# Optimization experiments

Hardware: AMD Instinct MI355X
Metric: run time of the kernel (lower is better)

Reference implementation:

```python
import jax, jax.numpy as jnp
import numpy as np

IN_FEATURES = 256
OUT_FEATURES = 256
GRID_SIZE = 5
SPLINE_ORDER = 3
GRID_RANGE = (-1.0, 1.0)
LN_EPS = 1e-5


def _make_grid():
    h = (GRID_RANGE[1] - GRID_RANGE[0]) / GRID_SIZE
    n_knots = GRID_SIZE + 2 * SPLINE_ORDER + 1  # 12
    return jnp.linspace(GRID_RANGE[0] - h * SPLINE_ORDER,
                        GRID_RANGE[1] + h * SPLINE_ORDER,
                        n_knots, dtype=jnp.float32)


def setup_inputs() -> dict:
    key = jax.random.key(0)
    k1, k2, k3 = jax.random.split(key, 3)
    N = 65536
    # kaiming_uniform_(nonlinearity='linear'): bound = sqrt(3/fan_in)
    b1 = np.sqrt(3.0 / IN_FEATURES)
    fan_sp = IN_FEATURES * (GRID_SIZE + SPLINE_ORDER)
    b2 = np.sqrt(3.0 / fan_sp)
    return {
        "x": jax.random.normal(k1, (N, IN_FEATURES), dtype=jnp.float32),
        "grid": _make_grid(),
        "base_weight": jax.random.uniform(k2, (OUT_FEATURES, IN_FEATURES), jnp.float32, -b1, b1),
        "spline_weight": jax.random.uniform(k3, (OUT_FEATURES, IN_FEATURES, GRID_SIZE + SPLINE_ORDER), jnp.float32, -b2, b2),
        "ln_gamma": jnp.ones((OUT_FEATURES,), jnp.float32),
        "ln_beta": jnp.zeros((OUT_FEATURES,), jnp.float32),
        "prelu_a": jnp.full((1,), 0.25, jnp.float32),
    }


def reference(x, grid, base_weight, spline_weight, ln_gamma, ln_beta, prelu_a):
    # base branch: exact GELU then linear (matches nn.GELU() + F.linear)
    base_out = jnp.einsum('ni,oi->no', jax.nn.gelu(x, approximate=False), base_weight)

    # Cox-de Boor B-spline basis recursion. grid is identical per feature in
    # the original ([in, 12] expand of a 1D linspace) so we broadcast the 1D grid.
    xu = x[:, :, None]                                   # [N, in, 1]
    bases = ((xu >= grid[:-1]) & (xu < grid[1:])).astype(x.dtype)  # [N, in, 11]
    for k in range(1, SPLINE_ORDER + 1):
        left = grid[:-(k + 1)]
        right = grid[k:-1]
        delta = jnp.where(right == left, jnp.ones_like(right), right - left)
        bases = ((xu - left) / delta * bases[:, :, :-1]
                 + (grid[k + 1:] - xu) / (grid[k + 1:] - grid[1:-k]) * bases[:, :, 1:])
    # bases: [N, in, grid_size + spline_order]

    spline_out = jnp.einsum('nig,oig->no', bases, spline_weight)

    y = base_out + spline_out
    mu = jnp.mean(y, axis=-1, keepdims=True)
    var = jnp.mean(jnp.square(y - mu), axis=-1, keepdims=True)
    y = (y - mu) * jax.lax.rsqrt(var + LN_EPS) * ln_gamma + ln_beta
    # PReLU with a single shared slope (nn.PReLU default)
    return jnp.where(y >= 0, y, prelu_a[0] * y)
```

## Files before the change

### kernel.cpp

```cpp
#include <hip/hip_runtime.h>
#include <hip/hip_bf16.h>
#include <math.h>
#include <stdint.h>

typedef __attribute__((ext_vector_type(8))) short short8;
typedef __attribute__((ext_vector_type(8))) unsigned short u16x8;
typedef __attribute__((ext_vector_type(4))) float f32x4;

#define BM 256
#define BK 64
#define NKT 36
#define A_BYTES (BM * 128)
#define W_BYTES (256 * 128)
#define LDS_TOTAL (2 * A_BYTES + 2 * W_BYTES)

__device__ __forceinline__ unsigned short f2bf(float f) {
    union { float f; unsigned u; } c; c.f = f;
    unsigned u = c.u;
    unsigned r = u + 0x7fffu + ((u >> 16) & 1u);
    return (unsigned short)(r >> 16);
}

__device__ __forceinline__ float gelu_exact(float x) {
    return 0.5f * x * (1.0f + erff(x * 0.7071067811865475f));
}

__device__ __forceinline__ int swz(int row, int u) {
    return row * 128 + ((u ^ (row & 7)) << 4);
}

__global__ void kan_prep_w(const float* __restrict__ bw, const float* __restrict__ sw,
                           unsigned short* __restrict__ Ws) {
    int U = blockIdx.x * 256 + threadIdx.x;
    if (U >= NKT * 2048) return;
    int kt = U >> 11, lu = U & 2047;
    int row = lu >> 3, s = lu & 7;
    int uu = s ^ (row & 7);
    int k = kt * 64 + uu * 8;
    u16x8 pk;
#pragma unroll
    for (int e = 0; e < 8; ++e) {
        int kk = k + e;
        float v = (kk < 256) ? bw[row * 256 + kk] : sw[row * 2048 + (kk - 256)];
        pk[e] = f2bf(v);
    }
    *(u16x8*)(Ws + (size_t)U * 8) = pk;
}

__device__ __forceinline__ void w_issue(int kt, unsigned char* ldsWbuf,
                                        const unsigned short* __restrict__ Wshuf,
                                        int wid, int lane) {
    const unsigned short* wsrc = Wshuf + ((size_t)kt * 2048 + wid * 256 + lane) * 8;
    unsigned char* wdst = ldsWbuf + wid * 4096;
#pragma unroll
    for (int r = 0; r < 4; ++r) {
        __builtin_amdgcn_global_load_lds(
            (const __attribute__((address_space(1))) void*)(wsrc + r * 512),
            (__attribute__((address_space(3))) void*)(wdst + r * 1024),
            16, 0, 0);
    }
}

__device__ __forceinline__ u16x8 spline_row(float xv) {
    float xi = (xv + 2.2f) * 2.5f;
    float fi = floorf(xi);
    float tt = xi - fi;
    float s1 = 1.0f - tt;
    float t2 = tt * tt, t3 = t2 * tt;
    float w0 = s1 * s1 * s1 * (1.0f / 6.0f);
    float w1 = 0.5f * t3 - t2 + (2.0f / 3.0f);
    float w2 = -0.5f * t3 + 0.5f * t2 + 0.5f * tt + (1.0f / 6.0f);
    float w3 = t3 * (1.0f / 6.0f);
    uint64_t Wp = (uint64_t)f2bf(w0) | ((uint64_t)f2bf(w1) << 16)
                | ((uint64_t)f2bf(w2) << 32) | ((uint64_t)f2bf(w3) << 48);
    int b = 16 * ((int)fi - 3);
    uint64_t L = (b >= 0 && b < 64) ? (Wp << b)
               : ((b < 0 && b > -64) ? (Wp >> (-b)) : 0ull);
    uint64_t H = (b >= 64 && b < 128) ? (Wp << (b - 64))
               : ((b > 0 && b < 64) ? (Wp >> (64 - b)) : 0ull);
    union { uint64_t q[2]; u16x8 v; } rr;
    rr.q[0] = L; rr.q[1] = H;
    return rr.v;
}

__global__ __launch_bounds__(512, 2) void kan_fused(
    const float* __restrict__ X, const unsigned short* __restrict__ Wshuf,
    const float* __restrict__ gamma, const float* __restrict__ beta,
    const float* __restrict__ prelu_a, float* __restrict__ OUT)
{
    extern __shared__ __align__(16) unsigned char lds[];

    const int t = threadIdx.x;
    const int row0 = blockIdx.x * BM;
    const int wid = t >> 6, lane = t & 63;
    const int wr = wid >> 2, wc = wid & 3;
    const int lcol = lane & 15, q = lane >> 4;
    const int srow = t >> 3, scol = t & 7;

    f32x4 acc[8][4];
#pragma unroll
    for (int m = 0; m < 8; ++m)
#pragma unroll
        for (int n = 0; n < 4; ++n) acc[m][n] = (f32x4){0.f, 0.f, 0.f, 0.f};

    w_issue(0, lds + 2 * A_BYTES, Wshuf, wid, lane);
    {
        float xg[32];
#pragma unroll
        for (int rep = 0; rep < 4; ++rep) {
            const float* xp = X + (size_t)(row0 + srow + rep * 64) * 256 + scol * 8;
            float4 v0 = *(const float4*)xp;
            float4 v1 = *(const float4*)(xp + 4);
            xg[rep * 8 + 0] = v0.x; xg[rep * 8 + 1] = v0.y; xg[rep * 8 + 2] = v0.z; xg[rep * 8 + 3] = v0.w;
            xg[rep * 8 + 4] = v1.x; xg[rep * 8 + 5] = v1.y; xg[rep * 8 + 6] = v1.z; xg[rep * 8 + 7] = v1.w;
        }
#pragma unroll
        for (int rep = 0; rep < 4; ++rep) {
            u16x8 pk;
#pragma unroll
            for (int j = 0; j < 8; ++j) pk[j] = f2bf(gelu_exact(xg[rep * 8 + j]));
            *(u16x8*)(lds + swz(srow + rep * 64, scol)) = pk;
        }
    }
    __syncthreads();

    for (int kt = 0; kt < NKT; ++kt) {
        const int cur = kt & 1;
        unsigned char* A_cur = lds + cur * A_BYTES;
        unsigned char* W_cur = lds + 2 * A_BYTES + cur * W_BYTES;
        unsigned char* A_nxt = lds + (cur ^ 1) * A_BYTES;
        unsigned char* W_nxt = lds + 2 * A_BYTES + (cur ^ 1) * W_BYTES;
        const bool has_next = (kt + 1 < NKT);
        const bool nxt_gelu = (kt + 1 < 4);

        float xg[32]; float xs[4];
        if (has_next) {
            if (nxt_gelu) {
#pragma unroll
                for (int rep = 0; rep < 4; ++rep) {
                    const float* xp = X + (size_t)(row0 + srow + rep * 64) * 256
                                    + (kt + 1) * 64 + scol * 8;
                    float4 v0 = *(const float4*)xp;
                    float4 v1 = *(const float4*)(xp + 4);
                    xg[rep * 8 + 0] = v0.x; xg[rep * 8 + 1] = v0.y; xg[rep * 8 + 2] = v0.z; xg[rep * 8 + 3] = v0.w;
                    xg[rep * 8 + 4] = v1.x; xg[rep * 8 + 5] = v1.y; xg[rep * 8 + 6] = v1.z; xg[rep * 8 + 7] = v1.w;
                }
            } else {
                const int ibase = (kt + 1 - 4) * 8;
#pragma unroll
                for (int rep = 0; rep < 4; ++rep)
                    xs[rep] = X[(size_t)(row0 + srow + rep * 64) * 256 + ibase + scol];
            }
            w_issue(kt + 1, W_nxt, Wshuf, wid, lane);
        }

        short8 af[8], bfr[4];
#pragma unroll
        for (int m = 0; m < 8; ++m)
            af[m] = *(const short8*)(A_cur + swz(wr * 128 + m * 16 + lcol, q));
#pragma unroll
        for (int n = 0; n < 4; ++n)
            bfr[n] = *(const short8*)(W_cur + swz(wc * 64 + n * 16 + lcol, q));
#pragma unroll
        for (int m = 0; m < 8; ++m)
#pragma unroll
            for (int n = 0; n < 4; ++n)
                acc[m][n] = __builtin_amdgcn_mfma_f32_16x16x32_bf16(
                    af[m], bfr[n], acc[m][n], 0, 0, 0);
#pragma unroll
        for (int m = 0; m < 8; ++m)
            af[m] = *(const short8*)(A_cur + swz(wr * 128 + m * 16 + lcol, 4 + q));
#pragma unroll
        for (int n = 0; n < 4; ++n)
            bfr[n] = *(const short8*)(W_cur + swz(wc * 64 + n * 16 + lcol, 4 + q));
#pragma unroll
        for (int m = 0; m < 8; ++m)
#pragma unroll
            for (int n = 0; n < 4; ++n)
                acc[m][n] = __builtin_amdgcn_mfma_f32_16x16x32_bf16(
                    af[m], bfr[n], acc[m][n], 0, 0, 0);

        if (has_next) {
            if (nxt_gelu) {
#pragma unroll
                for (int rep = 0; rep < 4; ++rep) {
                    u16x8 pk;
#pragma unroll
                    for (int j = 0; j < 8; ++j) pk[j] = f2bf(gelu_exact(xg[rep * 8 + j]));
                    *(u16x8*)(A_nxt + swz(srow + rep * 64, scol)) = pk;
                }
            } else {
#pragma unroll
                for (int rep = 0; rep < 4; ++rep)
                    *(u16x8*)(A_nxt + swz(srow + rep * 64, scol)) = spline_row(xs[rep]);
            }
        }
        __syncthreads();
    }

    float* stats = (float*)lds;
#pragma unroll
    for (int m = 0; m < 8; ++m) {
#pragma unroll
        for (int r = 0; r < 4; ++r) {
            float s = 0.f, s2 = 0.f;
#pragma unroll
            for (int n = 0; n < 4; ++n) { float v = acc[m][n][r]; s += v; s2 += v * v; }
#pragma unroll
            for (int msk = 1; msk < 16; msk <<= 1) {
                s  += __shfl_xor(s,  msk, 64);
                s2 += __shfl_xor(s2, msk, 64);
            }
            if ((lane & 15) == ((m * 4 + r) & 15)) {
                int row = wr * 128 + m * 16 + q * 4 + r;
                stats[row * 8 + wc]     = s;
                stats[row * 8 + 4 + wc] = s2;
            }
        }
    }
    __syncthreads();

    const float apr = prelu_a[0];
    float gv[4], bv[4];
#pragma unroll
    for (int n = 0; n < 4; ++n) {
        int col = wc * 64 + n * 16 + lcol;
        gv[n] = gamma[col]; bv[n] = beta[col];
    }
#pragma unroll
    for (int m = 0; m < 8; ++m) {
#pragma unroll
        for (int r = 0; r < 4; ++r) {
            int row = wr * 128 + m * 16 + q * 4 + r;
            f32x4 sv = *(const f32x4*)(stats + row * 8);
            f32x4 qv = *(const f32x4*)(stats + row * 8 + 4);
            float mu  = (sv[0] + sv[1] + sv[2] + sv[3]) * (1.0f / 256.0f);
            float ex2 = (qv[0] + qv[1] + qv[2] + qv[3]) * (1.0f / 256.0f);
            float rs = rsqrtf(ex2 - mu * mu + 1e-5f);
            float* op = OUT + (size_t)(row0 + row) * 256;
#pragma unroll
            for (int n = 0; n < 4; ++n) {
                int col = wc * 64 + n * 16 + lcol;
                float y = (acc[m][n][r] - mu) * rs * gv[n] + bv[n];
                op[col] = (y >= 0.f) ? y : apr * y;
            }
        }
    }
}

extern "C" void kernel_launch(void* const* d_in, const int* in_sizes, int n_in,
                              void* d_out, int out_size, void* d_ws, size_t ws_size,
                              hipStream_t stream) {
    const float* x  = (const float*)d_in[0];
    const float* bw = (const float*)d_in[2];
    const float* sw = (const float*)d_in[3];
    const float* g  = (const float*)d_in[4];
    const float* be = (const float*)d_in[5];
    const float* pa = (const float*)d_in[6];
    float* out = (float*)d_out;
    unsigned short* Ws = (unsigned short*)d_ws;

    hipFuncSetAttribute((const void*)kan_fused,
                        hipFuncAttributeMaxDynamicSharedMemorySize, LDS_TOTAL);

    const int Nrows = in_sizes[0] / 256;
    kan_prep_w<<<(NKT * 2048 + 255) / 256, 256, 0, stream>>>(bw, sw, Ws);
    kan_fused<<<Nrows / BM, 512, LDS_TOTAL, stream>>>(x, Ws, g, be, pa, out);
}
```

Before: 136.4 us.

## Load weight fragments directly into registers, dropping LDS staging for W

The prep kernel now writes weights in MFMA fragment order, so each wave loads its B operands straight from global memory into registers, double-buffered across k-tiles. The W LDS buffers and the global_load_lds path are removed, which halves LDS use and removes the B-side LDS reads. __syncthreads is replaced by a raw lgkmcnt wait plus s_barrier. The costs are more register pressure (16 short8 buffers on top of 32 accumulators) and a global-load latency sitting inside each iteration. The raw barrier does not wait on vmcnt, so correctness depends on the compiler placing waits before the register-held weights are used.

```diff
diff --git a/kernel.cpp b/kernel.cpp
--- a/kernel.cpp
+++ b/kernel.cpp
@@ -4,15 +4,12 @@
 #include <stdint.h>
 
 typedef __attribute__((ext_vector_type(8))) short short8;
-typedef __attribute__((ext_vector_type(8))) unsigned short u16x8;
 typedef __attribute__((ext_vector_type(4))) float f32x4;
 
 #define BM 256
-#define BK 64
 #define NKT 36
 #define A_BYTES (BM * 128)
-#define W_BYTES (256 * 128)
-#define LDS_TOTAL (2 * A_BYTES + 2 * W_BYTES)
+#define LDS_TOTAL (2 * A_BYTES)
 
 __device__ __forceinline__ unsigned short f2bf(float f) {
     union { float f; unsigned u; } c; c.f = f;
@@ -30,38 +27,26 @@
 }
 
 __global__ void kan_prep_w(const float* __restrict__ bw, const float* __restrict__ sw,
-                           unsigned short* __restrict__ Ws) {
+                           unsigned short* __restrict__ Wf) {
     int U = blockIdx.x * 256 + threadIdx.x;
     if (U >= NKT * 2048) return;
-    int kt = U >> 11, lu = U & 2047;
-    int row = lu >> 3, s = lu & 7;
-    int uu = s ^ (row & 7);
-    int k = kt * 64 + uu * 8;
-    u16x8 pk;
+    int kt = U >> 11, rem = U & 2047;
+    int wcq = rem >> 9, rem2 = rem & 511;
+    int i = rem2 >> 6;
+    int lane = rem2 & 63;
+    int o = wcq * 64 + (i & 3) * 16 + (lane & 15);
+    int k0 = kt * 64 + ((i >> 2) * 4 + (lane >> 4)) * 8;
+    unsigned short pk[8];
 #pragma unroll
     for (int e = 0; e < 8; ++e) {
-        int kk = k + e;
-        float v = (kk < 256) ? bw[row * 256 + kk] : sw[row * 2048 + (kk - 256)];
+        int kk = k0 + e;
+        float v = (kk < 256) ? bw[o * 256 + kk] : sw[o * 2048 + (kk - 256)];
         pk[e] = f2bf(v);
     }
-    *(u16x8*)(Ws + (size_t)U * 8) = pk;
-}
-
-__device__ __forceinline__ void w_issue(int kt, unsigned char* ldsWbuf,
-                                        const unsigned short* __restrict__ Wshuf,
-                                        int wid, int lane) {
-    const unsigned short* wsrc = Wshuf + ((size_t)kt * 2048 + wid * 256 + lane) * 8;
-    unsigned char* wdst = ldsWbuf + wid * 4096;
-#pragma unroll
-    for (int r = 0; r < 4; ++r) {
-        __builtin_amdgcn_global_load_lds(
-            (const __attribute__((address_space(1))) void*)(wsrc + r * 512),
-            (__attribute__((address_space(3))) void*)(wdst + r * 1024),
-            16, 0, 0);
-    }
-}
-
-__device__ __forceinline__ u16x8 spline_row(float xv) {
+    *(short8*)(Wf + (size_t)U * 8) = *(short8*)pk;
+}
+
+__device__ __forceinline__ short8 spline_row(float xv) {
     float xi = (xv + 2.2f) * 2.5f;
     float fi = floorf(xi);
     float tt = xi - fi;
@@ -78,13 +63,13 @@
                : ((b < 0 && b > -64) ? (Wp >> (-b)) : 0ull);
     uint64_t H = (b >= 64 && b < 128) ? (Wp << (b - 64))
                : ((b > 0 && b < 64) ? (Wp >> (64 - b)) : 0ull);
-    union { uint64_t q[2]; u16x8 v; } rr;
+    union { uint64_t q[2]; short8 v; } rr;
     rr.q[0] = L; rr.q[1] = H;
     return rr.v;
 }
 
 __global__ __launch_bounds__(512, 2) void kan_fused(
-    const float* __restrict__ X, const unsigned short* __restrict__ Wshuf,
+    const float* __restrict__ X, const unsigned short* __restrict__ Wf,
     const float* __restrict__ gamma, const float* __restrict__ beta,
     const float* __restrict__ prelu_a, float* __restrict__ OUT)
 {
@@ -103,33 +88,30 @@
 #pragma unroll
         for (int n = 0; n < 4; ++n) acc[m][n] = (f32x4){0.f, 0.f, 0.f, 0.f};
 
-    w_issue(0, lds + 2 * A_BYTES, Wshuf, wid, lane);
+    const unsigned short* wlane = Wf + ((size_t)wc * 512 + lane) * 8;
+
+    short8 wvA[8], wvB[8];
+#pragma unroll
+    for (int i = 0; i < 8; ++i)
+        wvA[i] = *(const short8*)(wlane + i * 512);
     {
-        float xg[32];
 #pragma unroll
         for (int rep = 0; rep < 4; ++rep) {
             const float* xp = X + (size_t)(row0 + srow + rep * 64) * 256 + scol * 8;
             float4 v0 = *(const float4*)xp;
             float4 v1 = *(const float4*)(xp + 4);
-            xg[rep * 8 + 0] = v0.x; xg[rep * 8 + 1] = v0.y; xg[rep * 8 + 2] = v0.z; xg[rep * 8 + 3] = v0.w;
-            xg[rep * 8 + 4] = v1.x; xg[rep * 8 + 5] = v1.y; xg[rep * 8 + 6] = v1.z; xg[rep * 8 + 7] = v1.w;
-        }
-#pragma unroll
-        for (int rep = 0; rep < 4; ++rep) {
-            u16x8 pk;
-#pragma unroll
-            for (int j = 0; j < 8; ++j) pk[j] = f2bf(gelu_exact(xg[rep * 8 + j]));
-            *(u16x8*)(lds + swz(srow + rep * 64, scol)) = pk;
-        }
-    }
-    __syncthreads();
-
-    for (int kt = 0; kt < NKT; ++kt) {
-        const int cur = kt & 1;
-        unsigned char* A_cur = lds + cur * A_BYTES;
-        unsigned char* W_cur = lds + 2 * A_BYTES + cur * W_BYTES;
-        unsigned char* A_nxt = lds + (cur ^ 1) * A_BYTES;
-        unsigned char* W_nxt = lds + 2 * A_BYTES + (cur ^ 1) * W_BYTES;
+            float vv[8] = {v0.x, v0.y, v0.z, v0.w, v1.x, v1.y, v1.z, v1.w};
+            unsigned short pk[8];
+#pragma unroll
+            for (int j = 0; j < 8; ++j) pk[j] = f2bf(gelu_exact(vv[j]));
+            *(short8*)(lds + swz(srow + rep * 64, scol)) = *(short8*)pk;
+        }
+    }
+    asm volatile("s_waitcnt lgkmcnt(0)\n\ts_barrier" ::: "memory");
+
+    auto body = [&](int kt, short8 (&wv)[8], short8 (&wn)[8]) {
+        unsigned char* A_cur = lds + (kt & 1) * A_BYTES;
+        unsigned char* A_nxt = lds + ((kt + 1) & 1) * A_BYTES;
         const bool has_next = (kt + 1 < NKT);
         const bool nxt_gelu = (kt + 1 < 4);
 
@@ -142,8 +124,10 @@
                                     + (kt + 1) * 64 + scol * 8;
                     float4 v0 = *(const float4*)xp;
                     float4 v1 = *(const float4*)(xp + 4);
-                    xg[rep * 8 + 0] = v0.x; xg[rep * 8 + 1] = v0.y; xg[rep * 8 + 2] = v0.z; xg[rep * 8 + 3] = v0.w;
-                    xg[rep * 8 + 4] = v1.x; xg[rep * 8 + 5] = v1.y; xg[rep * 8 + 6] = v1.z; xg[rep * 8 + 7] = v1.w;
+                    xg[rep * 8 + 0] = v0.x; xg[rep * 8 + 1] = v0.y;
+                    xg[rep * 8 + 2] = v0.z; xg[rep * 8 + 3] = v0.w;
+                    xg[rep * 8 + 4] = v1.x; xg[rep * 8 + 5] = v1.y;
+                    xg[rep * 8 + 6] = v1.z; xg[rep * 8 + 7] = v1.w;
                 }
             } else {
                 const int ibase = (kt + 1 - 4) * 8;
@@ -151,51 +135,47 @@
                 for (int rep = 0; rep < 4; ++rep)
                     xs[rep] = X[(size_t)(row0 + srow + rep * 64) * 256 + ibase + scol];
             }
-            w_issue(kt + 1, W_nxt, Wshuf, wid, lane);
-        }
-
-        short8 af[8], bfr[4];
-#pragma unroll
-        for (int m = 0; m < 8; ++m)
-            af[m] = *(const short8*)(A_cur + swz(wr * 128 + m * 16 + lcol, q));
-#pragma unroll
-        for (int n = 0; n < 4; ++n)
-            bfr[n] = *(const short8*)(W_cur + swz(wc * 64 + n * 16 + lcol, q));
-#pragma unroll
-        for (int m = 0; m < 8; ++m)
-#pragma unroll
-            for (int n = 0; n < 4; ++n)
-                acc[m][n] = __builtin_amdgcn_mfma_f32_16x16x32_bf16(
-                    af[m], bfr[n], acc[m][n], 0, 0, 0);
-#pragma unroll
-        for (int m = 0; m < 8; ++m)
-            af[m] = *(const short8*)(A_cur + swz(wr * 128 + m * 16 + lcol, 4 + q));
-#pragma unroll
-        for (int n = 0; n < 4; ++n)
-            bfr[n] = *(const short8*)(W_cur + swz(wc * 64 + n * 16 + lcol, 4 + q));
-#pragma unroll
-        for (int m = 0; m < 8; ++m)
-#pragma unroll
-            for (int n = 0; n < 4; ++n)
-                acc[m][n] = __builtin_amdgcn_mfma_f32_16x16x32_bf16(
-                    af[m], bfr[n], acc[m][n], 0, 0, 0);
+            const unsigned short* wsrc = wlane + (size_t)(kt + 1) * 2048 * 8;
+#pragma unroll
+            for (int i = 0; i < 8; ++i)
+                wn[i] = *(const short8*)(wsrc + i * 512);
+        }
+
+#pragma unroll
+        for (int kh = 0; kh < 2; ++kh) {
+            short8 af[8];
+#pragma unroll
+            for (int m = 0; m < 8; ++m)
+                af[m] = *(const short8*)(A_cur + swz(wr * 128 + m * 16 + lcol, kh * 4 + q));
+#pragma unroll
+            for (int m = 0; m < 8; ++m)
+#pragma unroll
+                for (int n = 0; n < 4; ++n)
+                    acc[m][n] = __builtin_amdgcn_mfma_f32_16x16x32_bf16(
+                        af[m], wv[kh * 4 + n], acc[m][n], 0, 0, 0);
+        }
 
         if (has_next) {
             if (nxt_gelu) {
 #pragma unroll
                 for (int rep = 0; rep < 4; ++rep) {
-                    u16x8 pk;
+                    unsigned short pk[8];
 #pragma unroll
                     for (int j = 0; j < 8; ++j) pk[j] = f2bf(gelu_exact(xg[rep * 8 + j]));
-                    *(u16x8*)(A_nxt + swz(srow + rep * 64, scol)) = pk;
+                    *(short8*)(A_nxt + swz(srow + rep * 64, scol)) = *(short8*)pk;
                 }
             } else {
 #pragma unroll
                 for (int rep = 0; rep < 4; ++rep)
-                    *(u16x8*)(A_nxt + swz(srow + rep * 64, scol)) = spline_row(xs[rep]);
-            }
-        }
-        __syncthreads();
+                    *(short8*)(A_nxt + swz(srow + rep * 64, scol)) = spline_row(xs[rep]);
+            }
+        }
+        asm volatile("s_waitcnt lgkmcnt(0)\n\ts_barrier" ::: "memory");
+    };
+
+    for (int kp = 0; kp < NKT; kp += 2) {
+        body(kp,     wvA, wvB);
+        body(kp + 1, wvB, wvA);
     }
 
     float* stats = (float*)lds;
@@ -258,12 +238,12 @@
     const float* be = (const float*)d_in[5];
     const float* pa = (const float*)d_in[6];
     float* out = (float*)d_out;
-    unsigned short* Ws = (unsigned short*)d_ws;
+    unsigned short* Wf = (unsigned short*)d_ws;
 
     hipFuncSetAttribute((const void*)kan_fused,
                         hipFuncAttributeMaxDynamicSharedMemorySize, LDS_TOTAL);
 
     const int Nrows = in_sizes[0] / 256;
-    kan_prep_w<<<(NKT * 2048 + 255) / 256, 256, 0, stream>>>(bw, sw, Ws);
-    kan_fused<<<Nrows / BM, 512, LDS_TOTAL, stream>>>(x, Ws, g, be, pa, out);
-}
+    kan_prep_w<<<(NKT * 2048 + 255) / 256, 256, 0, stream>>>(bw, sw, Wf);
+    kan_fused<<<Nrows / BM, 512, LDS_TOTAL, stream>>>(x, Wf, g, be, pa, out);
+}
```

After: 196.3 us. 1.44x slower.
